# Kernel optimization log

Measured on AMD Instinct MI355X. Metric: run time of the kernel, lower is better.

## Reference

```python
import jax, jax.numpy as jnp
import numpy as np

B, T, D, R = 4, 1024, 512, 64
SLOTS = (1024, 256, 64)
K = 16


def _layernorm(x, g, b, eps=1e-5):
    m = jnp.mean(x, axis=-1, keepdims=True)
    v = jnp.mean(jnp.square(x - m), axis=-1, keepdims=True)
    return (x - m) * jax.lax.rsqrt(v + eps) * g + b


def _signed_softmax(x):
    # signed softmax over the slot axis: sign(x) * softmax(|x|)
    return jnp.sign(x) * jax.nn.softmax(jnp.abs(x), axis=-1)


def _transition_delta(src_val, src_state, dst_val, W, k, n_dst):
    # Low-rank bilinear routing: logits [B, Ns, Nd]
    q = jnp.einsum('bsd,dr->bsr', src_val, W[0])
    kk = jnp.einsum('bnd,dr->bnr', dst_val, W[1])
    logits = jnp.einsum('bsr,bnr->bsn', q, kk) / jnp.sqrt(jnp.float32(W.shape[-1]))
    v, idx = jax.lax.top_k(logits, k)                      # [B, Ns, k]
    w = jnp.sign(v) * jax.nn.softmax(jnp.abs(v), axis=-1)  # signed_abs_softmax over selected edges
    c = w * jax.nn.softplus(src_state)[:, :, None]         # state-weighted edge coefficients [B, Ns, k]
    d = src_val.shape[-1]
    edge_val = (c[..., None] * src_val[:, :, None, :]).reshape(src_val.shape[0], -1, d)
    idx_f = idx.reshape(idx.shape[0], -1)
    cf = c.reshape(c.shape[0], -1)

    def _scatter(i, ev, cc):
        dv = jnp.zeros((n_dst, d), src_val.dtype).at[i].add(ev)
        ds = jnp.zeros((n_dst,), src_val.dtype).at[i].add(cc)
        return ds, dv

    return jax.vmap(_scatter)(idx_f, edge_val, cf)


def _apply_delta(state, val, dstate, dval, g, b):
    # residual merge, then constrain: signed softmax state + LayerNorm values
    return _signed_softmax(state + dstate), _layernorm(val + dval, g, b)


def setup_inputs() -> dict:
    key = jax.random.key(0)
    ks = jax.random.split(key, 20)
    rn = lambda k, s, sc=1.0: jax.random.normal(k, s, jnp.float32) * sc
    return {
        'tok_val': rn(ks[0], (B, T, D)),
        'tok_state': rn(ks[1], (B, T)),
        'mem_state0': rn(ks[2], (B, SLOTS[0]), 0.02),
        'mem_val0': rn(ks[3], (B, SLOTS[0], D), 0.02),
        'mem_state1': rn(ks[4], (B, SLOTS[1]), 0.02),
        'mem_val1': rn(ks[5], (B, SLOTS[1], D), 0.02),
        'mem_state2': rn(ks[6], (B, SLOTS[2]), 0.02),
        'mem_val2': rn(ks[7], (B, SLOTS[2], D), 0.02),
        'write_route': rn(ks[8], (1, 2, D, R), 0.05),
        'prop_route': rn(ks[9], (3, 2, D, R), 0.05),
        'level_route': rn(ks[10], (2, 2, D, R), 0.05),
        'skip_route': rn(ks[11], (2, 2, D, R), 0.05),
        'skip_gates': jnp.full((2,), -1.5, jnp.float32),
        'ln_gamma': jnp.ones((3, D), jnp.float32),
        'ln_beta': jnp.zeros((3, D), jnp.float32),
        'read_route': rn(ks[12], (3, 2, D, R), 0.05),
        'read_proj': rn(ks[13], (3, D, D), 0.02),
        'read_gates': jnp.zeros((3,), jnp.float32),
        'topk': K,
    }


def reference(tok_val, tok_state, mem_state0, mem_val0, mem_state1, mem_val1,
              mem_state2, mem_val2, write_route, prop_route, level_route,
              skip_route, skip_gates, ln_gamma, ln_beta, read_route, read_proj,
              read_gates, topk):
    k = int(topk)
    S0, S1, S2 = mem_state0.shape[1], mem_state1.shape[1], mem_state2.shape[1]

    # --- level 0: token write + pairwise propagation ---
    ds, dv = _transition_delta(tok_val, tok_state, mem_val0, write_route[0], min(k, S0), S0)
    s0, v0 = _apply_delta(mem_state0, mem_val0, ds, dv, ln_gamma[0], ln_beta[0])
    ds, dv = _transition_delta(v0, s0, v0, prop_route[0], min(k, S0), S0)
    s0, v0 = _apply_delta(s0, v0, ds, dv, ln_gamma[0], ln_beta[0])

    # --- level 1: transition from level 0, gated skip from tokens, propagation ---
    ds, dv = _transition_delta(v0, s0, mem_val1, level_route[0], min(k, S1), S1)
    s1, v1 = _apply_delta(mem_state1, mem_val1, ds, dv, ln_gamma[1], ln_beta[1])
    g = jax.nn.sigmoid(skip_gates[0])
    ds, dv = _transition_delta(tok_val, tok_state, v1, skip_route[0], min(k, S1), S1)
    s1, v1 = _apply_delta(s1, v1, g * ds, g * dv, ln_gamma[1], ln_beta[1])
    ds, dv = _transition_delta(v1, s1, v1, prop_route[1], min(k, S1), S1)
    s1, v1 = _apply_delta(s1, v1, ds, dv, ln_gamma[1], ln_beta[1])

    # --- level 2: transition from level 1, gated skip from level 0, propagation ---
    ds, dv = _transition_delta(v1, s1, mem_val2, level_route[1], min(k, S2), S2)
    s2, v2 = _apply_delta(mem_state2, mem_val2, ds, dv, ln_gamma[2], ln_beta[2])
    g = jax.nn.sigmoid(skip_gates[1])
    ds, dv = _transition_delta(v0, s0, v2, skip_route[1], min(k, S2), S2)
    s2, v2 = _apply_delta(s2, v2, g * ds, g * dv, ln_gamma[2], ln_beta[2])
    ds, dv = _transition_delta(v2, s2, v2, prop_route[2], min(k, S2), S2)
    s2, v2 = _apply_delta(s2, v2, ds, dv, ln_gamma[2], ln_beta[2])

    # --- read: tokens attend over each memory level, gated projected residual ---
    out = tok_val
    for l, mv in enumerate((v0, v1, v2)):
        q = jnp.einsum('btd,dr->btr', tok_val, read_route[l, 0])
        kk = jnp.einsum('bnd,dr->bnr', mv, read_route[l, 1])
        logits = jnp.einsum('btr,bnr->btn', q, kk) / jnp.sqrt(jnp.float32(R))
        attn = jax.nn.softmax(logits, axis=-1)
        r = jnp.einsum('btn,bnd->btd', attn, mv)
        out = out + jax.nn.sigmoid(read_gates[l]) * jnp.einsum('btd,de->bte', r, read_proj[l])
    return out
```

## Files before the change

kernel.cpp:

```cpp
#include <hip/hip_runtime.h>
#include <math.h>

typedef __attribute__((ext_vector_type(8))) short short8;
typedef __attribute__((ext_vector_type(4))) float floatx4;

static __device__ __forceinline__ short f2bf(float f) {
    union { float f; unsigned u; } c; c.f = f;
    unsigned r = c.u + 0x7FFF + ((c.u >> 16) & 1);
    return (short)(r >> 16);
}

__launch_bounds__(256)
__global__ void gemm_f32_nt_kernel(const float* __restrict__ A, const float* __restrict__ B,
                                   float* __restrict__ C, int M, int N, int K,
                                   long sA, long sB, long sC, float alpha)
{
    __shared__ float As[32][68];
    __shared__ float Bs[32][68];
    const float* Ab = A + (long)blockIdx.z * sA;
    const float* Bb = B + (long)blockIdx.z * sB;
    float* Cb = C + (long)blockIdx.z * sC;
    int m0 = blockIdx.x * 64, n0 = blockIdx.y * 64;
    int t = threadIdx.x;
    int tx = t & 15, ty = t >> 4;
    float acc[4][4] = {};

    for (int k0 = 0; k0 < K; k0 += 32) {
        {
            int m = t >> 3;
            int kk = (t & 7) * 4;
#pragma unroll
            for (int h = 0; h < 2; ++h) {
                float4 v = *(const float4*)&Ab[(long)(m0 + m + 32 * h) * K + k0 + kk];
                As[kk + 0][m + 32 * h] = v.x; As[kk + 1][m + 32 * h] = v.y;
                As[kk + 2][m + 32 * h] = v.z; As[kk + 3][m + 32 * h] = v.w;
            }
        }
        {
            int n = t >> 3;
            int kk = (t & 7) * 4;
#pragma unroll
            for (int h = 0; h < 2; ++h) {
                float4 v = *(const float4*)&Bb[(long)(n0 + n + 32 * h) * K + k0 + kk];
                Bs[kk + 0][n + 32 * h] = v.x; Bs[kk + 1][n + 32 * h] = v.y;
                Bs[kk + 2][n + 32 * h] = v.z; Bs[kk + 3][n + 32 * h] = v.w;
            }
        }
        __syncthreads();
#pragma unroll 4
        for (int k = 0; k < 32; ++k) {
            float4 a = *(const float4*)&As[k][ty * 4];
            float4 b = *(const float4*)&Bs[k][tx * 4];
            float av[4] = { a.x, a.y, a.z, a.w };
            float bv[4] = { b.x, b.y, b.z, b.w };
#pragma unroll
            for (int i = 0; i < 4; ++i)
#pragma unroll
                for (int j = 0; j < 4; ++j) acc[i][j] += av[i] * bv[j];
        }
        __syncthreads();
    }
#pragma unroll
    for (int i = 0; i < 4; ++i) {
        float4 r;
        r.x = alpha * acc[i][0]; r.y = alpha * acc[i][1];
        r.z = alpha * acc[i][2]; r.w = alpha * acc[i][3];
        *(float4*)&Cb[(long)(m0 + ty * 4 + i) * N + n0 + tx * 4] = r;
    }
}

__launch_bounds__(256)
__global__ void proj_splitk_kernel(const float* __restrict__ Aq, const float* __restrict__ Ak,
                                   const float* __restrict__ Wq, const float* __restrict__ Wk,
                                   float* __restrict__ part,
                                   int Mq, int Mk, long sAq, long sAk, int Bn)
{
    __shared__ float As[32][68];
    __shared__ float Bs[32][68];
    int mqT = Mq >> 6;
    int xt = blockIdx.x, s = blockIdx.y, b = blockIdx.z;
    const float* A; const float* W; int row0, orow;
    if (xt < mqT) { A = Aq + (long)b * sAq; W = Wq; row0 = xt * 64; orow = row0; }
    else { A = Ak + (long)b * sAk; W = Wk; row0 = (xt - mqT) * 64; orow = Mq + row0; }
    int t = threadIdx.x, tx = t & 15, ty = t >> 4;
    float acc[4][4] = {};
    int kbase = s * 64;

    for (int k0 = kbase; k0 < kbase + 64; k0 += 32) {
        {
            int m = t >> 3;
            int kk = (t & 7) * 4;
#pragma unroll
            for (int h = 0; h < 2; ++h) {
                float4 v = *(const float4*)&A[(long)(row0 + m + 32 * h) * 512 + k0 + kk];
                As[kk + 0][m + 32 * h] = v.x; As[kk + 1][m + 32 * h] = v.y;
                As[kk + 2][m + 32 * h] = v.z; As[kk + 3][m + 32 * h] = v.w;
            }
        }
        {
            int kk = t >> 3;
            int nn = (t & 7) * 8;
            float4 v0 = *(const float4*)&W[(long)(k0 + kk) * 64 + nn];
            float4 v1 = *(const float4*)&W[(long)(k0 + kk) * 64 + nn + 4];
            *(float4*)&Bs[kk][nn] = v0;
            *(float4*)&Bs[kk][nn + 4] = v1;
        }
        __syncthreads();
#pragma unroll 4
        for (int k = 0; k < 32; ++k) {
            float4 a = *(const float4*)&As[k][ty * 4];
            float4 b2 = *(const float4*)&Bs[k][tx * 4];
            float av[4] = { a.x, a.y, a.z, a.w };
            float bv[4] = { b2.x, b2.y, b2.z, b2.w };
#pragma unroll
            for (int i = 0; i < 4; ++i)
#pragma unroll
                for (int j = 0; j < 4; ++j) acc[i][j] += av[i] * bv[j];
        }
        __syncthreads();
    }
    long base = ((long)(s * Bn + b) * (Mq + Mk) + orow) * 64;
#pragma unroll
    for (int i = 0; i < 4; ++i)
        *(float4*)&part[base + (long)(ty * 4 + i) * 64 + tx * 4] =
            make_float4(acc[i][0], acc[i][1], acc[i][2], acc[i][3]);
}

__launch_bounds__(256)
__global__ void proj_reduce_kernel(const float* __restrict__ part,
                                   float* __restrict__ qout, float* __restrict__ kout,
                                   int Mq, int Mk, int Bn)
{
    int idx = blockIdx.x * 256 + threadIdx.x;
    int size4b = (Mq + Mk) * 16;
    int total4 = Bn * size4b;
    if (idx >= total4) return;
    const float4* p4 = (const float4*)part;
    long stride4 = (long)total4;
    float4 s = p4[idx];
#pragma unroll
    for (int ss = 1; ss < 8; ++ss) {
        float4 v = p4[ss * stride4 + idx];
        s.x += v.x; s.y += v.y; s.z += v.z; s.w += v.w;
    }
    int b = idx / size4b;
    int rem = idx - b * size4b;
    int r = rem >> 4;
    int c4 = rem & 15;
    if (r < Mq) ((float4*)qout)[((long)b * Mq + r) * 16 + c4] = s;
    else        ((float4*)kout)[((long)b * Mk + (r - Mq)) * 16 + c4] = s;
}

struct ProjDesc {
    const float* A[6];
    const float* W[6];
    long  sA[6];
    int   tileOff[7];
    int   rowOff[6];
    int   Mtot;
};

__launch_bounds__(256)
__global__ void proj_splitk_multi_kernel(ProjDesc d, float* __restrict__ part, int Bn)
{
    __shared__ float As[32][68];
    __shared__ float Bs[32][68];
    int xt = blockIdx.x, s = blockIdx.y, b = blockIdx.z;
    int seg = 0;
    while (xt >= d.tileOff[seg + 1]) ++seg;
    int row0 = (xt - d.tileOff[seg]) * 64;
    const float* A = d.A[seg] + (long)b * d.sA[seg];
    const float* W = d.W[seg];
    int orow = d.rowOff[seg] + row0;
    int t = threadIdx.x, tx = t & 15, ty = t >> 4;
    float acc[4][4] = {};
    int kbase = s * 64;

    for (int k0 = kbase; k0 < kbase + 64; k0 += 32) {
        {
            int m = t >> 3;
            int kk = (t & 7) * 4;
#pragma unroll
            for (int h = 0; h < 2; ++h) {
                float4 v = *(const float4*)&A[(long)(row0 + m + 32 * h) * 512 + k0 + kk];
                As[kk + 0][m + 32 * h] = v.x; As[kk + 1][m + 32 * h] = v.y;
                As[kk + 2][m + 32 * h] = v.z; As[kk + 3][m + 32 * h] = v.w;
            }
        }
        {
            int kk = t >> 3;
            int nn = (t & 7) * 8;
            float4 v0 = *(const float4*)&W[(long)(k0 + kk) * 64 + nn];
            float4 v1 = *(const float4*)&W[(long)(k0 + kk) * 64 + nn + 4];
            *(float4*)&Bs[kk][nn] = v0;
            *(float4*)&Bs[kk][nn + 4] = v1;
        }
        __syncthreads();
#pragma unroll 4
        for (int k = 0; k < 32; ++k) {
            float4 a = *(const float4*)&As[k][ty * 4];
            float4 b2 = *(const float4*)&Bs[k][tx * 4];
            float av[4] = { a.x, a.y, a.z, a.w };
            float bv[4] = { b2.x, b2.y, b2.z, b2.w };
#pragma unroll
            for (int i = 0; i < 4; ++i)
#pragma unroll
                for (int j = 0; j < 4; ++j) acc[i][j] += av[i] * bv[j];
        }
        __syncthreads();
    }
    long base = ((long)(s * Bn + b) * d.Mtot + orow) * 64;
#pragma unroll
    for (int i = 0; i < 4; ++i)
        *(float4*)&part[base + (long)(ty * 4 + i) * 64 + tx * 4] =
            make_float4(acc[i][0], acc[i][1], acc[i][2], acc[i][3]);
}

__launch_bounds__(256)
__global__ void proj_reduce_flat_kernel(const float* __restrict__ part, float* __restrict__ outp,
                                        int total4)
{
    int idx = blockIdx.x * 256 + threadIdx.x;
    if (idx >= total4) return;
    const float4* p4 = (const float4*)part;
    float4 s = p4[idx];
#pragma unroll
    for (int ss = 1; ss < 8; ++ss) {
        float4 v = p4[(long)ss * total4 + idx];
        s.x += v.x; s.y += v.y; s.z += v.z; s.w += v.w;
    }
    ((float4*)outp)[idx] = s;
}

__launch_bounds__(256)
__global__ void gemm_mfma_kernel(const float* __restrict__ A, const unsigned short* __restrict__ Bt,
                                 float* __restrict__ C, int M, int N, int K,
                                 long sA, long sBt, long sC,
                                 float alpha, const float* __restrict__ gate, int gateIdx,
                                 float beta, const float* __restrict__ initC)
{
    __shared__ short As[2048];
    __shared__ short Bs[2048];
    const float* Ab = A + (long)blockIdx.z * sA;
    const unsigned short* Bb = Bt + (long)blockIdx.z * sBt;
    float* Cb = C + (long)blockIdx.z * sC;
    const float* Ib = initC ? initC + (long)blockIdx.z * sC : nullptr;
    int m0 = blockIdx.x * 64, n0 = blockIdx.y * 64;
    int t = threadIdx.x, wave = t >> 6, lane = t & 63;
    int sr = wave * 16 + (lane & 15);
    int sk = (lane >> 4) * 8;
    floatx4 acc[4] = {};

    for (int k0 = 0; k0 < K; k0 += 32) {
        const float* ap = &Ab[(long)(m0 + sr) * K + k0 + sk];
        float4 f0 = *(const float4*)ap;
        float4 f1 = *(const float4*)(ap + 4);
        short8 av;
        av[0] = f2bf(f0.x); av[1] = f2bf(f0.y); av[2] = f2bf(f0.z); av[3] = f2bf(f0.w);
        av[4] = f2bf(f1.x); av[5] = f2bf(f1.y); av[6] = f2bf(f1.z); av[7] = f2bf(f1.w);
        short8 bv = *(const short8*)&Bb[(long)(n0 + sr) * K + k0 + sk];
        ((short8*)As)[t] = av;
        ((short8*)Bs)[t] = bv;
        __syncthreads();
        short8 bf = ((short8*)Bs)[wave * 64 + lane];
#pragma unroll
        for (int mt = 0; mt < 4; ++mt) {
            short8 af = ((short8*)As)[mt * 64 + lane];
            acc[mt] = __builtin_amdgcn_mfma_f32_16x16x32_bf16(af, bf, acc[mt], 0, 0, 0);
        }
        __syncthreads();
    }
    float a = alpha;
    if (gate) a *= 1.f / (1.f + expf(-gate[gateIdx]));
    int col = n0 + wave * 16 + (lane & 15);
#pragma unroll
    for (int mt = 0; mt < 4; ++mt) {
#pragma unroll
        for (int r = 0; r < 4; ++r) {
            int row = m0 + mt * 16 + (lane >> 4) * 4 + r;
            long off = (long)row * N + col;
            float v = a * acc[mt][r];
            if (Ib) v += Ib[off];
            else if (beta != 0.f) v += Cb[off];
            Cb[off] = v;
        }
    }
}

__global__ void transpose_bf16_kernel(const float* __restrict__ in, unsigned short* __restrict__ out,
                                      int Rr, int Cc, long sIn, long sOut)
{
    __shared__ float tile[32][33];
    const float* I = in + (long)blockIdx.z * sIn;
    unsigned short* O = out + (long)blockIdx.z * sOut;
    int c0 = blockIdx.x * 32, r0 = blockIdx.y * 32;
    int tx = threadIdx.x, ty = threadIdx.y;
#pragma unroll
    for (int i = 0; i < 32; i += 8)
        tile[ty + i][tx] = I[(long)(r0 + ty + i) * Cc + c0 + tx];
    __syncthreads();
#pragma unroll
    for (int i = 0; i < 32; i += 8)
        O[(long)(c0 + ty + i) * Rr + r0 + tx] = (unsigned short)f2bf(tile[tx][ty + i]);
}

__global__ void transpose_mv_kernel(const float* __restrict__ mv0, const float* __restrict__ mv1,
                                    const float* __restrict__ mv2,
                                    unsigned short* __restrict__ o0, unsigned short* __restrict__ o1,
                                    unsigned short* __restrict__ o2)
{
    __shared__ float tile[32][33];
    int yt = blockIdx.y;
    const float* in; unsigned short* out; int Nd, r0t;
    if (yt < 32)      { in = mv0; out = o0; Nd = 1024; r0t = yt; }
    else if (yt < 40) { in = mv1; out = o1; Nd = 256;  r0t = yt - 32; }
    else              { in = mv2; out = o2; Nd = 64;   r0t = yt - 40; }
    const float* I = in + (long)blockIdx.z * Nd * 512;
    unsigned short* O = out + (long)blockIdx.z * 512 * Nd;
    int c0 = blockIdx.x * 32, r0 = r0t * 32;
    int tx = threadIdx.x, ty = threadIdx.y;
#pragma unroll
    for (int i = 0; i < 32; i += 8)
        tile[ty + i][tx] = I[(long)(r0 + ty + i) * 512 + c0 + tx];
    __syncthreads();
#pragma unroll
    for (int i = 0; i < 32; i += 8)
        O[(long)(c0 + ty + i) * Nd + r0 + tx] = (unsigned short)f2bf(tile[tx][ty + i]);
}

template<int CNT>
__launch_bounds__(256)
__global__ void topk_coeff_kernel(const float* __restrict__ logits,
                                  const float* __restrict__ state,
                                  int* __restrict__ idx_out, float* __restrict__ c_out,
                                  int* __restrict__ cnt, int nsLog, int Nd)
{
    int wave = threadIdx.x >> 6, lane = threadIdx.x & 63;
    long row = (long)blockIdx.x * 4 + wave;
    const float* L = logits + row * Nd;
    float vreg[CNT];
    if (CNT >= 4) {
#pragma unroll
        for (int q = 0; q < CNT / 4; ++q) {
            float4 v = *(const float4*)&L[lane * CNT + q * 4];
            vreg[q * 4 + 0] = v.x; vreg[q * 4 + 1] = v.y;
            vreg[q * 4 + 2] = v.z; vreg[q * 4 + 3] = v.w;
        }
    } else {
#pragma unroll
        for (int tt = 0; tt < CNT; ++tt) vreg[tt] = L[lane * CNT + tt];
    }

    float m = 0.f, sum = 0.f;
    float myv = 0.f; int myi = 0;
#pragma unroll
    for (int it = 0; it < 16; ++it) {
        float best = -INFINITY; int bidx = 0x7fffffff;
#pragma unroll
        for (int tt = 0; tt < CNT; ++tt) {
            if (vreg[tt] > best) { best = vreg[tt]; bidx = lane * CNT + tt; }
        }
#pragma unroll
        for (int off = 32; off; off >>= 1) {
            float ov = __shfl_down(best, off);
            int   oi = __shfl_down(bidx, off);
            if (ov > best || (ov == best && oi < bidx)) { best = ov; bidx = oi; }
        }
        best = __shfl(best, 0);
        bidx = __shfl(bidx, 0);
        if (it == lane) { myv = best; myi = bidx; }
        float ab = fabsf(best);
        float nm = fmaxf(m, ab);
        sum = sum * expf(m - nm) + expf(ab - nm);
        m = nm;
#pragma unroll
        for (int tt = 0; tt < CNT; ++tt)
            if (lane * CNT + tt == bidx) vreg[tt] = -INFINITY;
    }
    if (lane < 16) {
        float st = state[row];
        float sp = fmaxf(st, 0.f) + log1pf(expf(-fabsf(st)));
        float sgn = (myv > 0.f) ? 1.f : ((myv < 0.f) ? -1.f : 0.f);
        float w = expf(fabsf(myv) - m) / sum;
        c_out[row * 16 + lane] = sgn * w * sp;
        idx_out[row * 16 + lane] = myi;
        int b = (int)(row >> nsLog);
        atomicAdd(&cnt[b * Nd + myi], 1);
    }
}

__launch_bounds__(256)
__global__ void scan_kernel(int* __restrict__ cnt, int* __restrict__ offs, int N)
{
    __shared__ int sums[256];
    int t = threadIdx.x;
    int chunk = N >> 8;
    int base = t * chunk;
    int lc[16];
    int s = 0;
    for (int i = 0; i < chunk; ++i) { lc[i] = cnt[base + i]; s += lc[i]; }
    sums[t] = s;
    __syncthreads();
    for (int off = 1; off < 256; off <<= 1) {
        int v = (t >= off) ? sums[t - off] : 0;
        __syncthreads();
        sums[t] += v;
        __syncthreads();
    }
    int run = sums[t] - s;
    for (int i = 0; i < chunk; ++i) {
        offs[base + i] = run;
        run += lc[i];
        cnt[base + i] = 0;
    }
    if (t == 255) offs[N] = run;
}

__launch_bounds__(256)
__global__ void fill_edges_kernel(const int* __restrict__ idx, const int* __restrict__ offs,
                                  int* __restrict__ cursor, int* __restrict__ elist,
                                  int nsShift, int Nd, int E)
{
    int e = blockIdx.x * 256 + threadIdx.x;
    if (e >= E) return;
    int b = e >> nsShift;
    int d = b * Nd + idx[e];
    int pos = offs[d] + atomicAdd(&cursor[d], 1);
    elist[pos] = e;
}

#define ECHUNK 512
__launch_bounds__(256)
__global__ void gather_ln_kernel(const float* __restrict__ src_val, const float* __restrict__ c,
                                 const int* __restrict__ elist, const int* __restrict__ offs,
                                 const float* __restrict__ v_in, float* __restrict__ v_out,
                                 float* __restrict__ ds, int* __restrict__ cursor,
                                 const float* __restrict__ gamma, const float* __restrict__ beta,
                                 const float* __restrict__ gatePtr, int gateIdx, int nsShift)
{
    __shared__ float sc[ECHUNK];
    __shared__ int   srow[ECHUNK];
    __shared__ float part[4][512];
    __shared__ float pcs[4];
    __shared__ float red[4];
    long row = blockIdx.x;
    int t = threadIdx.x, w = t >> 6, lane = t & 63;
    int e0 = offs[row], e1 = offs[row + 1];
    int mask = (1 << nsShift) - 1;
    int cb = lane * 8;
    float a[8] = {};
    float cs = 0.f;
    float gate = 1.f;
    if (gatePtr) gate = 1.f / (1.f + expf(-gatePtr[gateIdx]));

    for (int cstart = e0; cstart < e1; cstart += ECHUNK) {
        int cnt = min(e1 - cstart, ECHUNK);
        for (int i = t; i < cnt; i += 256) {
            int e = elist[cstart + i];
            sc[i] = c[e];
            int b = e >> nsShift;
            int s = (e & mask) >> 4;
            srow[i] = (b << (nsShift - 4)) + s;
        }
        __syncthreads();
        int j = w;
        for (; j + 12 < cnt; j += 16) {
            float c0 = sc[j], c1 = sc[j + 4], c2 = sc[j + 8], c3 = sc[j + 12];
            const float* p0 = src_val + ((long)srow[j]      << 9) + cb;
            const float* p1 = src_val + ((long)srow[j + 4]  << 9) + cb;
            const float* p2 = src_val + ((long)srow[j + 8]  << 9) + cb;
            const float* p3 = src_val + ((long)srow[j + 12] << 9) + cb;
            float4 x00 = *(const float4*)p0,       x01 = *(const float4*)(p0 + 4);
            float4 x10 = *(const float4*)p1,       x11 = *(const float4*)(p1 + 4);
            float4 x20 = *(const float4*)p2,       x21 = *(const float4*)(p2 + 4);
            float4 x30 = *(const float4*)p3,       x31 = *(const float4*)(p3 + 4);
            a[0] += c0 * x00.x + c1 * x10.x + c2 * x20.x + c3 * x30.x;
            a[1] += c0 * x00.y + c1 * x10.y + c2 * x20.y + c3 * x30.y;
            a[2] += c0 * x00.z + c1 * x10.z + c2 * x20.z + c3 * x30.z;
            a[3] += c0 * x00.w + c1 * x10.w + c2 * x20.w + c3 * x30.w;
            a[4] += c0 * x01.x + c1 * x11.x + c2 * x21.x + c3 * x31.x;
            a[5] += c0 * x01.y + c1 * x11.y + c2 * x21.y + c3 * x31.y;
            a[6] += c0 * x01.z + c1 * x11.z + c2 * x21.z + c3 * x31.z;
            a[7] += c0 * x01.w + c1 * x11.w + c2 * x21.w + c3 * x31.w;
            cs += c0 + c1 + c2 + c3;
        }
        for (; j < cnt; j += 4) {
            float cv = sc[j];
            const float* p = src_val + ((long)srow[j] << 9) + cb;
            float4 x0 = *(const float4*)p, x1 = *(const float4*)(p + 4);
            a[0] += cv * x0.x; a[1] += cv * x0.y; a[2] += cv * x0.z; a[3] += cv * x0.w;
            a[4] += cv * x1.x; a[5] += cv * x1.y; a[6] += cv * x1.z; a[7] += cv * x1.w;
            cs += cv;
        }
        __syncthreads();
    }
#pragma unroll
    for (int i = 0; i < 8; ++i) part[w][cb + i] = a[i];
    if (lane == 0) pcs[w] = cs;
    __syncthreads();
    float r0 = part[0][t] + part[1][t] + part[2][t] + part[3][t];
    float r1 = part[0][t + 256] + part[1][t + 256] + part[2][t + 256] + part[3][t + 256];
    if (t == 0) { ds[row] = pcs[0] + pcs[1] + pcs[2] + pcs[3]; cursor[row] = 0; }

    const float* vi = v_in + (row << 9);
    float x0 = vi[t]       + gate * r0;
    float x1 = vi[t + 256] + gate * r1;
    float s = x0 + x1;
    for (int off = 32; off; off >>= 1) s += __shfl_down(s, off);
    if ((t & 63) == 0) red[t >> 6] = s;
    __syncthreads();
    float mean = (red[0] + red[1] + red[2] + red[3]) * (1.f / 512.f);
    float d0 = x0 - mean, d1 = x1 - mean;
    float ss = d0 * d0 + d1 * d1;
    for (int off = 32; off; off >>= 1) ss += __shfl_down(ss, off);
    __syncthreads();
    if ((t & 63) == 0) red[t >> 6] = ss;
    __syncthreads();
    float var = (red[0] + red[1] + red[2] + red[3]) * (1.f / 512.f);
    float rstd = rsqrtf(var + 1e-5f);
    float* vo = v_out + (row << 9);
    vo[t]       = d0 * rstd * gamma[t]       + beta[t];
    vo[t + 256] = d1 * rstd * gamma[t + 256] + beta[t + 256];
}

__launch_bounds__(256)
__global__ void apply_state_kernel(const float* __restrict__ s_in, const float* __restrict__ ds,
                                   float* __restrict__ s_out, int Nd,
                                   const float* __restrict__ gatePtr, int gateIdx)
{
    __shared__ float sh[1024];
    __shared__ float red[4];
    int b = blockIdx.x, t = threadIdx.x;
    float gate = 1.f;
    if (gatePtr) gate = 1.f / (1.f + expf(-gatePtr[gateIdx]));
    float lmax = 0.f;
    for (int i = t; i < Nd; i += 256) {
        float x = s_in[b * Nd + i] + gate * ds[b * Nd + i];
        sh[i] = x;
        lmax = fmaxf(lmax, fabsf(x));
    }
    for (int off = 32; off; off >>= 1) lmax = fmaxf(lmax, __shfl_down(lmax, off));
    if ((t & 63) == 0) red[t >> 6] = lmax;
    __syncthreads();
    float bmax = fmaxf(fmaxf(red[0], red[1]), fmaxf(red[2], red[3]));
    float lsum = 0.f;
    for (int i = t; i < Nd; i += 256) lsum += expf(fabsf(sh[i]) - bmax);
    for (int off = 32; off; off >>= 1) lsum += __shfl_down(lsum, off);
    __syncthreads();
    if ((t & 63) == 0) red[t >> 6] = lsum;
    __syncthreads();
    float inv = 1.f / (red[0] + red[1] + red[2] + red[3]);
    for (int i = t; i < Nd; i += 256) {
        float x = sh[i];
        float sgn = (x > 0.f) ? 1.f : ((x < 0.f) ? -1.f : 0.f);
        s_out[b * Nd + i] = sgn * expf(fabsf(x) - bmax) * inv;
    }
}

__launch_bounds__(256)
__global__ void softmax_rows_kernel(float* __restrict__ logits, int Nd)
{
    __shared__ float red[4];
    long row = blockIdx.x;
    int t = threadIdx.x;
    float* L = logits + row * (long)Nd;
    float lmax = -INFINITY;
    for (int i = t; i < Nd; i += 256) lmax = fmaxf(lmax, L[i]);
    for (int off = 32; off; off >>= 1) lmax = fmaxf(lmax, __shfl_down(lmax, off));
    if ((t & 63) == 0) red[t >> 6] = lmax;
    __syncthreads();
    float bmax = fmaxf(fmaxf(red[0], red[1]), fmaxf(red[2], red[3]));
    float lsum = 0.f;
    for (int i = t; i < Nd; i += 256) lsum += expf(L[i] - bmax);
    for (int off = 32; off; off >>= 1) lsum += __shfl_down(lsum, off);
    __syncthreads();
    if ((t & 63) == 0) red[t >> 6] = lsum;
    __syncthreads();
    float inv = 1.f / (red[0] + red[1] + red[2] + red[3]);
    for (int i = t; i < Nd; i += 256) L[i] = expf(L[i] - bmax) * inv;
}

extern "C" void kernel_launch(void* const* d_in, const int* in_sizes, int n_in,
                              void* d_out, int out_size, void* d_ws, size_t ws_size,
                              hipStream_t stream)
{
    const int Bn = 4, T = 1024, D = 512, R = 64;
    const int S0 = 1024, S1 = 256, S2 = 64;
    const long RT = (long)D * R;
    const int MR = 3 * T + S0 + S1 + S2;

    const float* tok_val    = (const float*)d_in[0];
    const float* tok_state  = (const float*)d_in[1];
    const float* mem_state0 = (const float*)d_in[2];
    const float* mem_val0   = (const float*)d_in[3];
    const float* mem_state1 = (const float*)d_in[4];
    const float* mem_val1   = (const float*)d_in[5];
    const float* mem_state2 = (const float*)d_in[6];
    const float* mem_val2   = (const float*)d_in[7];
    const float* write_route= (const float*)d_in[8];
    const float* prop_route = (const float*)d_in[9];
    const float* level_route= (const float*)d_in[10];
    const float* skip_route = (const float*)d_in[11];
    const float* skip_gates = (const float*)d_in[12];
    const float* ln_gamma   = (const float*)d_in[13];
    const float* ln_beta    = (const float*)d_in[14];
    const float* read_route = (const float*)d_in[15];
    const float* read_proj  = (const float*)d_in[16];
    const float* read_gates = (const float*)d_in[17];
    float* out = (float*)d_out;

    float* p = (float*)d_ws;
    float* v0  = p; p += (long)Bn * S0 * D;
    float* v0b = p; p += (long)Bn * S0 * D;
    float* s0  = p; p += Bn * S0;
    float* v1  = p; p += (long)Bn * S1 * D;
    float* v1b = p; p += (long)Bn * S1 * D;
    float* s1  = p; p += Bn * S1;
    float* v2  = p; p += (long)Bn * S2 * D;
    float* v2b = p; p += (long)Bn * S2 * D;
    float* s2  = p; p += Bn * S2;
    float* qb  = p; p += (long)Bn * T * R;
    float* kb  = p; p += (long)Bn * S0 * R;
    float* rqk = p; p += (long)Bn * MR * R;
    float* lb  = p; p += (long)Bn * T * S0;
    float* cbuf= p; p += (long)Bn * T * 16;
    int*   ib  = (int*)p; p += (long)Bn * T * 16;
    float* dsb = p; p += Bn * S0;
    float* rb  = p; p += (long)Bn * T * D;
    int* cntb  = (int*)p; p += Bn * S0;
    int* curb  = (int*)p; p += Bn * S0;
    int* offsb = (int*)p; p += Bn * S0 + 1;
    int* elistb= (int*)p; p += (long)Bn * T * 16;
    unsigned short* projT = (unsigned short*)p; p += (3 * (long)D * D) / 2 + 4;
    unsigned short* mvT0  = (unsigned short*)p; p += ((long)Bn * D * S0) / 2 + 4;
    unsigned short* mvT1  = (unsigned short*)p; p += ((long)Bn * D * S1) / 2 + 4;
    unsigned short* mvT2  = (unsigned short*)p; p += ((long)Bn * D * S2) / 2 + 4;
    float* partb = p; p += 8L * Bn * MR * R;

    auto proj = [&](const float* Aq, const float* Ak, const float* Wq, const float* Wk,
                    int Mq, int Mk, long sAq, long sAk, float* qout, float* kout) {
        proj_splitk_kernel<<<dim3((Mq + Mk) / 64, 8, Bn), 256, 0, stream>>>(
            Aq, Ak, Wq, Wk, partb, Mq, Mk, sAq, sAk, Bn);
        int total4 = Bn * (Mq + Mk) * 16;
        proj_reduce_kernel<<<(total4 + 255) / 256, 256, 0, stream>>>(
            partb, qout, kout, Mq, Mk, Bn);
    };

    hipMemsetAsync(cntb, 0, (size_t)2 * Bn * S0 * sizeof(int), stream);

    auto trans = [&](const float* sv, const float* ss, const float* dval,
                     const float* W, int Ns, int Nd,
                     const float* v_in, float* v_out, const float* sin, float* sout,
                     int lvl, const float* gptr, int gidx) {
        proj(sv, dval, W, W + RT, Ns, Nd, (long)Ns * D, (long)Nd * D, qb, kb);
        gemm_f32_nt_kernel<<<dim3(Ns / 64, Nd / 64, Bn), 256, 0, stream>>>(
            qb, kb, lb, Ns, Nd, R, (long)Ns * R, (long)Nd * R, (long)Ns * Nd, 0.125f);
        int nsLog = 31 - __builtin_clz((unsigned)Ns);
        int nsShift = nsLog + 4;
        int rowBlocks = Bn * Ns / 4;
        if (Nd == 1024)
            topk_coeff_kernel<16><<<rowBlocks, 256, 0, stream>>>(lb, ss, ib, cbuf, cntb, nsLog, Nd);
        else if (Nd == 256)
            topk_coeff_kernel<4><<<rowBlocks, 256, 0, stream>>>(lb, ss, ib, cbuf, cntb, nsLog, Nd);
        else
            topk_coeff_kernel<1><<<rowBlocks, 256, 0, stream>>>(lb, ss, ib, cbuf, cntb, nsLog, Nd);
        int E = Bn * Ns * 16;
        scan_kernel<<<1, 256, 0, stream>>>(cntb, offsb, Bn * Nd);
        fill_edges_kernel<<<(E + 255) / 256, 256, 0, stream>>>(ib, offsb, curb, elistb,
                                                               nsShift, Nd, E);
        gather_ln_kernel<<<Bn * Nd, 256, 0, stream>>>(sv, cbuf, elistb, offsb,
                                                      v_in, v_out, dsb, curb,
                                                      ln_gamma + lvl * D, ln_beta + lvl * D,
                                                      gptr, gidx, nsShift);
        apply_state_kernel<<<Bn, 256, 0, stream>>>(sin, dsb, sout, Nd, gptr, gidx);
    };

    trans(tok_val, tok_state, mem_val0, write_route, T, S0,
          mem_val0, v0, mem_state0, s0, 0, nullptr, 0);
    trans(v0, s0, v0, prop_route + 0 * 2 * RT, S0, S0,
          v0, v0b, s0, s0, 0, nullptr, 0);

    trans(v0b, s0, mem_val1, level_route + 0 * 2 * RT, S0, S1,
          mem_val1, v1, mem_state1, s1, 1, nullptr, 0);
    trans(tok_val, tok_state, v1, skip_route + 0 * 2 * RT, T, S1,
          v1, v1, s1, s1, 1, skip_gates, 0);
    trans(v1, s1, v1, prop_route + 1 * 2 * RT, S1, S1,
          v1, v1b, s1, s1, 1, nullptr, 0);

    trans(v1b, s1, mem_val2, level_route + 1 * 2 * RT, S1, S2,
          mem_val2, v2, mem_state2, s2, 2, nullptr, 0);
    trans(v0b, s0, v2, skip_route + 1 * 2 * RT, S0, S2,
          v2, v2, s2, s2, 2, skip_gates, 1);
    trans(v2, s2, v2, prop_route + 2 * 2 * RT, S2, S2,
          v2, v2b, s2, s2, 2, nullptr, 0);

    transpose_bf16_kernel<<<dim3(D / 32, D / 32, 3), dim3(32, 8), 0, stream>>>(
        read_proj, projT, D, D, (long)D * D, (long)D * D);
    transpose_mv_kernel<<<dim3(D / 32, (S0 + S1 + S2) / 32, Bn), dim3(32, 8), 0, stream>>>(
        v0b, v1b, v2b, mvT0, mvT1, mvT2);

    {
        ProjDesc d = {};
        const float* mvs[3] = { v0b, v1b, v2b };
        const int nds[3] = { S0, S1, S2 };
        int tiles = 0, roff = 0;
        for (int l = 0; l < 3; ++l) {
            d.A[l] = tok_val; d.W[l] = read_route + (long)l * 2 * RT;
            d.sA[l] = (long)T * D; d.rowOff[l] = roff;
            d.tileOff[l] = tiles; tiles += T / 64; roff += T;
        }
        for (int l = 0; l < 3; ++l) {
            d.A[3 + l] = mvs[l]; d.W[3 + l] = read_route + (long)l * 2 * RT + RT;
            d.sA[3 + l] = (long)nds[l] * D; d.rowOff[3 + l] = roff;
            d.tileOff[3 + l] = tiles; tiles += nds[l] / 64; roff += nds[l];
        }
        d.tileOff[6] = tiles;
        d.Mtot = MR;
        proj_splitk_multi_kernel<<<dim3(tiles, 8, Bn), 256, 0, stream>>>(d, partb, Bn);
        int total4 = Bn * MR * 16;
        proj_reduce_flat_kernel<<<(total4 + 255) / 256, 256, 0, stream>>>(partb, rqk, total4);
    }

    const unsigned short* mvTs[3] = { mvT0, mvT1, mvT2 };
    const int nds[3] = { S0, S1, S2 };
    int koff = 3 * T;
    for (int l = 0; l < 3; ++l) {
        int Nd = nds[l];
        gemm_f32_nt_kernel<<<dim3(T / 64, Nd / 64, Bn), 256, 0, stream>>>(
            rqk + (long)l * T * R, rqk + (long)koff * R, lb, T, Nd, R,
            (long)MR * R, (long)MR * R, (long)T * Nd, 0.125f);
        koff += Nd;
        softmax_rows_kernel<<<Bn * T, 256, 0, stream>>>(lb, Nd);
        gemm_mfma_kernel<<<dim3(T / 64, D / 64, Bn), 256, 0, stream>>>(
            lb, mvTs[l], rb, T, D, Nd, (long)T * Nd, (long)D * Nd, (long)T * D,
            1.f, nullptr, 0, 0.f, nullptr);
        gemm_mfma_kernel<<<dim3(T / 64, D / 64, Bn), 256, 0, stream>>>(
            rb, projT + (long)l * D * D, out, T, D, D,
            (long)T * D, 0, (long)T * D, 1.f, read_gates, l,
            1.f, (l == 0) ? tok_val : nullptr);
    }
}
```

Baseline: 909.0 us.

## Batch read-phase levels into segmented kernels and one concatenated projection GEMM

The per-level read loop of logits GEMM, softmax, attention GEMM and projection GEMM is replaced by single segmented launches covering all three memory levels. The attention outputs are concatenated along the feature axis, and the three gated projections are folded into one K=1536 GEMM whose weights are pre-scaled by the sigmoid gates. This cuts kernel launches and the read-modify-write accumulation into the output. It needs separate logits buffers per level and a larger concatenated intermediate, and the attention kernel has unbalanced work per block because K differs across levels.

```diff
diff --git a/kernel.cpp b/kernel.cpp
--- a/kernel.cpp
+++ b/kernel.cpp
@@ -65,6 +65,78 @@
         float4 r;
         r.x = alpha * acc[i][0]; r.y = alpha * acc[i][1];
         r.z = alpha * acc[i][2]; r.w = alpha * acc[i][3];
+        *(float4*)&Cb[(long)(m0 + ty * 4 + i) * N + n0 + tx * 4] = r;
+    }
+}
+
+struct LogitsSeg {
+    const float* A[3];
+    const float* B[3];
+    float* C[3];
+    long sC[3];
+    int Nd[3];
+    int yOff[4];
+    long sAB;
+};
+
+__launch_bounds__(256)
+__global__ void gemm_logits_seg_kernel(LogitsSeg d)
+{
+    __shared__ float As[32][68];
+    __shared__ float Bs[32][68];
+    int yt = blockIdx.y;
+    int seg = 0;
+    while (yt >= d.yOff[seg + 1]) ++seg;
+    int n0 = (yt - d.yOff[seg]) * 64;
+    const float* Ab = d.A[seg] + (long)blockIdx.z * d.sAB;
+    const float* Bb = d.B[seg] + (long)blockIdx.z * d.sAB;
+    float* Cb = d.C[seg] + (long)blockIdx.z * d.sC[seg];
+    int N = d.Nd[seg];
+    int m0 = blockIdx.x * 64;
+    int t = threadIdx.x, tx = t & 15, ty = t >> 4;
+    float acc[4][4] = {};
+    const int K = 64;
+
+    for (int k0 = 0; k0 < K; k0 += 32) {
+        {
+            int m = t >> 3;
+            int kk = (t & 7) * 4;
+#pragma unroll
+            for (int h = 0; h < 2; ++h) {
+                float4 v = *(const float4*)&Ab[(long)(m0 + m + 32 * h) * K + k0 + kk];
+                As[kk + 0][m + 32 * h] = v.x; As[kk + 1][m + 32 * h] = v.y;
+                As[kk + 2][m + 32 * h] = v.z; As[kk + 3][m + 32 * h] = v.w;
+            }
+        }
+        {
+            int n = t >> 3;
+            int kk = (t & 7) * 4;
+#pragma unroll
+            for (int h = 0; h < 2; ++h) {
+                float4 v = *(const float4*)&Bb[(long)(n0 + n + 32 * h) * K + k0 + kk];
+                Bs[kk + 0][n + 32 * h] = v.x; Bs[kk + 1][n + 32 * h] = v.y;
+                Bs[kk + 2][n + 32 * h] = v.z; Bs[kk + 3][n + 32 * h] = v.w;
+            }
+        }
+        __syncthreads();
+#pragma unroll 4
+        for (int k = 0; k < 32; ++k) {
+            float4 a = *(const float4*)&As[k][ty * 4];
+            float4 b = *(const float4*)&Bs[k][tx * 4];
+            float av[4] = { a.x, a.y, a.z, a.w };
+            float bv[4] = { b.x, b.y, b.z, b.w };
+#pragma unroll
+            for (int i = 0; i < 4; ++i)
+#pragma unroll
+                for (int j = 0; j < 4; ++j) acc[i][j] += av[i] * bv[j];
+        }
+        __syncthreads();
+    }
+#pragma unroll
+    for (int i = 0; i < 4; ++i) {
+        float4 r;
+        r.x = 0.125f * acc[i][0]; r.y = 0.125f * acc[i][1];
+        r.z = 0.125f * acc[i][2]; r.w = 0.125f * acc[i][3];
         *(float4*)&Cb[(long)(m0 + ty * 4 + i) * N + n0 + tx * 4] = r;
     }
 }
@@ -236,8 +308,7 @@
 __global__ void gemm_mfma_kernel(const float* __restrict__ A, const unsigned short* __restrict__ Bt,
                                  float* __restrict__ C, int M, int N, int K,
                                  long sA, long sBt, long sC,
-                                 float alpha, const float* __restrict__ gate, int gateIdx,
-                                 float beta, const float* __restrict__ initC)
+                                 float alpha, const float* __restrict__ initC)
 {
     __shared__ short As[2048];
     __shared__ short Bs[2048];
@@ -270,8 +341,6 @@
         }
         __syncthreads();
     }
-    float a = alpha;
-    if (gate) a *= 1.f / (1.f + expf(-gate[gateIdx]));
     int col = n0 + wave * 16 + (lane & 15);
 #pragma unroll
     for (int mt = 0; mt < 4; ++mt) {
@@ -279,29 +348,85 @@
         for (int r = 0; r < 4; ++r) {
             int row = m0 + mt * 16 + (lane >> 4) * 4 + r;
             long off = (long)row * N + col;
-            float v = a * acc[mt][r];
+            float v = alpha * acc[mt][r];
             if (Ib) v += Ib[off];
-            else if (beta != 0.f) v += Cb[off];
             Cb[off] = v;
         }
     }
 }
 
-__global__ void transpose_bf16_kernel(const float* __restrict__ in, unsigned short* __restrict__ out,
-                                      int Rr, int Cc, long sIn, long sOut)
+struct AttnSeg {
+    const float* A[3];
+    const unsigned short* Bt[3];
+    int K[3];
+    long sA[3], sBt[3];
+};
+
+__launch_bounds__(256)
+__global__ void gemm_mfma_attn_seg_kernel(AttnSeg d, float* __restrict__ rcat, long sC)
+{
+    __shared__ short As[2048];
+    __shared__ short Bs[2048];
+    int lvl = blockIdx.x >> 4;
+    int m0 = (blockIdx.x & 15) * 64;
+    int n0 = blockIdx.y * 64;
+    int K = d.K[lvl];
+    const float* Ab = d.A[lvl] + (long)blockIdx.z * d.sA[lvl];
+    const unsigned short* Bb = d.Bt[lvl] + (long)blockIdx.z * d.sBt[lvl];
+    float* Cb = rcat + (long)blockIdx.z * sC + lvl * 512;
+    int t = threadIdx.x, wave = t >> 6, lane = t & 63;
+    int sr = wave * 16 + (lane & 15);
+    int sk = (lane >> 4) * 8;
+    floatx4 acc[4] = {};
+
+    for (int k0 = 0; k0 < K; k0 += 32) {
+        const float* ap = &Ab[(long)(m0 + sr) * K + k0 + sk];
+        float4 f0 = *(const float4*)ap;
+        float4 f1 = *(const float4*)(ap + 4);
+        short8 av;
+        av[0] = f2bf(f0.x); av[1] = f2bf(f0.y); av[2] = f2bf(f0.z); av[3] = f2bf(f0.w);
+        av[4] = f2bf(f1.x); av[5] = f2bf(f1.y); av[6] = f2bf(f1.z); av[7] = f2bf(f1.w);
+        short8 bv = *(const short8*)&Bb[(long)(n0 + sr) * K + k0 + sk];
+        ((short8*)As)[t] = av;
+        ((short8*)Bs)[t] = bv;
+        __syncthreads();
+        short8 bf = ((short8*)Bs)[wave * 64 + lane];
+#pragma unroll
+        for (int mt = 0; mt < 4; ++mt) {
+            short8 af = ((short8*)As)[mt * 64 + lane];
+            acc[mt] = __builtin_amdgcn_mfma_f32_16x16x32_bf16(af, bf, acc[mt], 0, 0, 0);
+        }
+        __syncthreads();
+    }
+    int col = n0 + wave * 16 + (lane & 15);
+#pragma unroll
+    for (int mt = 0; mt < 4; ++mt) {
+#pragma unroll
+        for (int r = 0; r < 4; ++r) {
+            int row = m0 + mt * 16 + (lane >> 4) * 4 + r;
+            Cb[(long)row * 1536 + col] = acc[mt][r];
+        }
+    }
+}
+
+__global__ void transpose_proj_gated_kernel(const float* __restrict__ proj,
+                                            const float* __restrict__ gates,
+                                            unsigned short* __restrict__ outp)
 {
     __shared__ float tile[32][33];
-    const float* I = in + (long)blockIdx.z * sIn;
-    unsigned short* O = out + (long)blockIdx.z * sOut;
-    int c0 = blockIdx.x * 32, r0 = blockIdx.y * 32;
+    int l = blockIdx.z;
+    float g = 1.f / (1.f + expf(-gates[l]));
+    const float* I = proj + (long)l * 512 * 512;
+    int n0 = blockIdx.x * 32, d0 = blockIdx.y * 32;
     int tx = threadIdx.x, ty = threadIdx.y;
 #pragma unroll
     for (int i = 0; i < 32; i += 8)
-        tile[ty + i][tx] = I[(long)(r0 + ty + i) * Cc + c0 + tx];
+        tile[ty + i][tx] = I[(long)(d0 + ty + i) * 512 + n0 + tx];
     __syncthreads();
 #pragma unroll
     for (int i = 0; i < 32; i += 8)
-        O[(long)(c0 + ty + i) * Rr + r0 + tx] = (unsigned short)f2bf(tile[tx][ty + i]);
+        outp[(long)(n0 + ty + i) * 1536 + l * 512 + d0 + tx] =
+            (unsigned short)f2bf(g * tile[tx][ty + i]);
 }
 
 __global__ void transpose_mv_kernel(const float* __restrict__ mv0, const float* __restrict__ mv1,
@@ -558,12 +683,16 @@
 }
 
 __launch_bounds__(256)
-__global__ void softmax_rows_kernel(float* __restrict__ logits, int Nd)
+__global__ void softmax_seg_kernel(float* __restrict__ lb0, float* __restrict__ lb1,
+                                   float* __restrict__ lb2)
 {
     __shared__ float red[4];
+    int lvl = blockIdx.y;
+    int Nd = (lvl == 0) ? 1024 : (lvl == 1) ? 256 : 64;
+    float* base = (lvl == 0) ? lb0 : (lvl == 1) ? lb1 : lb2;
     long row = blockIdx.x;
     int t = threadIdx.x;
-    float* L = logits + row * (long)Nd;
+    float* L = base + row * (long)Nd;
     float lmax = -INFINITY;
     for (int i = t; i < Nd; i += 256) lmax = fmaxf(lmax, L[i]);
     for (int off = 32; off; off >>= 1) lmax = fmaxf(lmax, __shfl_down(lmax, off));
@@ -622,16 +751,18 @@
     float* qb  = p; p += (long)Bn * T * R;
     float* kb  = p; p += (long)Bn * S0 * R;
     float* rqk = p; p += (long)Bn * MR * R;
-    float* lb  = p; p += (long)Bn * T * S0;
+    float* lb0 = p; p += (long)Bn * T * S0;
+    float* lb1 = p; p += (long)Bn * T * S1;
+    float* lb2 = p; p += (long)Bn * T * S2;
     float* cbuf= p; p += (long)Bn * T * 16;
     int*   ib  = (int*)p; p += (long)Bn * T * 16;
     float* dsb = p; p += Bn * S0;
-    float* rb  = p; p += (long)Bn * T * D;
+    float* rcat= p; p += (long)Bn * T * 1536;
     int* cntb  = (int*)p; p += Bn * S0;
     int* curb  = (int*)p; p += Bn * S0;
     int* offsb = (int*)p; p += Bn * S0 + 1;
     int* elistb= (int*)p; p += (long)Bn * T * 16;
-    unsigned short* projT = (unsigned short*)p; p += (3 * (long)D * D) / 2 + 4;
+    unsigned short* pcatT = (unsigned short*)p; p += (512L * 1536) / 2 + 4;
     unsigned short* mvT0  = (unsigned short*)p; p += ((long)Bn * D * S0) / 2 + 4;
     unsigned short* mvT1  = (unsigned short*)p; p += ((long)Bn * D * S1) / 2 + 4;
     unsigned short* mvT2  = (unsigned short*)p; p += ((long)Bn * D * S2) / 2 + 4;
@@ -654,16 +785,16 @@
                      int lvl, const float* gptr, int gidx) {
         proj(sv, dval, W, W + RT, Ns, Nd, (long)Ns * D, (long)Nd * D, qb, kb);
         gemm_f32_nt_kernel<<<dim3(Ns / 64, Nd / 64, Bn), 256, 0, stream>>>(
-            qb, kb, lb, Ns, Nd, R, (long)Ns * R, (long)Nd * R, (long)Ns * Nd, 0.125f);
+            qb, kb, lb0, Ns, Nd, R, (long)Ns * R, (long)Nd * R, (long)Ns * Nd, 0.125f);
         int nsLog = 31 - __builtin_clz((unsigned)Ns);
         int nsShift = nsLog + 4;
         int rowBlocks = Bn * Ns / 4;
         if (Nd == 1024)
-            topk_coeff_kernel<16><<<rowBlocks, 256, 0, stream>>>(lb, ss, ib, cbuf, cntb, nsLog, Nd);
+            topk_coeff_kernel<16><<<rowBlocks, 256, 0, stream>>>(lb0, ss, ib, cbuf, cntb, nsLog, Nd);
         else if (Nd == 256)
-            topk_coeff_kernel<4><<<rowBlocks, 256, 0, stream>>>(lb, ss, ib, cbuf, cntb, nsLog, Nd);
+            topk_coeff_kernel<4><<<rowBlocks, 256, 0, stream>>>(lb0, ss, ib, cbuf, cntb, nsLog, Nd);
         else
-            topk_coeff_kernel<1><<<rowBlocks, 256, 0, stream>>>(lb, ss, ib, cbuf, cntb, nsLog, Nd);
+            topk_coeff_kernel<1><<<rowBlocks, 256, 0, stream>>>(lb0, ss, ib, cbuf, cntb, nsLog, Nd);
         int E = Bn * Ns * 16;
         scan_kernel<<<1, 256, 0, stream>>>(cntb, offsb, Bn * Nd);
         fill_edges_kernel<<<(E + 255) / 256, 256, 0, stream>>>(ib, offsb, curb, elistb,
@@ -694,8 +825,8 @@
     trans(v2, s2, v2, prop_route + 2 * 2 * RT, S2, S2,
           v2, v2b, s2, s2, 2, nullptr, 0);
 
-    transpose_bf16_kernel<<<dim3(D / 32, D / 32, 3), dim3(32, 8), 0, stream>>>(
-        read_proj, projT, D, D, (long)D * D, (long)D * D);
+    transpose_proj_gated_kernel<<<dim3(D / 32, D / 32, 3), dim3(32, 8), 0, stream>>>(
+        read_proj, read_gates, pcatT);
     transpose_mv_kernel<<<dim3(D / 32, (S0 + S1 + S2) / 32, Bn), dim3(32, 8), 0, stream>>>(
         v0b, v1b, v2b, mvT0, mvT1, mvT2);
 
@@ -721,22 +852,45 @@
         proj_reduce_flat_kernel<<<(total4 + 255) / 256, 256, 0, stream>>>(partb, rqk, total4);
     }
 
-    const unsigned short* mvTs[3] = { mvT0, mvT1, mvT2 };
-    const int nds[3] = { S0, S1, S2 };
-    int koff = 3 * T;
-    for (int l = 0; l < 3; ++l) {
-        int Nd = nds[l];
-        gemm_f32_nt_kernel<<<dim3(T / 64, Nd / 64, Bn), 256, 0, stream>>>(
-            rqk + (long)l * T * R, rqk + (long)koff * R, lb, T, Nd, R,
-            (long)MR * R, (long)MR * R, (long)T * Nd, 0.125f);
-        koff += Nd;
-        softmax_rows_kernel<<<Bn * T, 256, 0, stream>>>(lb, Nd);
-        gemm_mfma_kernel<<<dim3(T / 64, D / 64, Bn), 256, 0, stream>>>(
-            lb, mvTs[l], rb, T, D, Nd, (long)T * Nd, (long)D * Nd, (long)T * D,
-            1.f, nullptr, 0, 0.f, nullptr);
-        gemm_mfma_kernel<<<dim3(T / 64, D / 64, Bn), 256, 0, stream>>>(
-            rb, projT + (long)l * D * D, out, T, D, D,
-            (long)T * D, 0, (long)T * D, 1.f, read_gates, l,
-            1.f, (l == 0) ? tok_val : nullptr);
-    }
-}
+    {
+        LogitsSeg d = {};
+        float* lbs[3] = { lb0, lb1, lb2 };
+        const int nds[3] = { S0, S1, S2 };
+        int koff = 3 * T, yo = 0;
+        for (int l = 0; l < 3; ++l) {
+            d.A[l] = rqk + (long)l * T * R;
+            d.B[l] = rqk + (long)koff * R;
+            d.C[l] = lbs[l];
+            d.sC[l] = (long)T * nds[l];
+            d.Nd[l] = nds[l];
+            d.yOff[l] = yo;
+            yo += nds[l] / 64;
+            koff += nds[l];
+        }
+        d.yOff[3] = yo;
+        d.sAB = (long)MR * R;
+        gemm_logits_seg_kernel<<<dim3(T / 64, yo, Bn), 256, 0, stream>>>(d);
+    }
+
+    softmax_seg_kernel<<<dim3(Bn * T, 3), 256, 0, stream>>>(lb0, lb1, lb2);
+
+    {
+        AttnSeg d = {};
+        float* lbs[3] = { lb0, lb1, lb2 };
+        const unsigned short* mvTs[3] = { mvT0, mvT1, mvT2 };
+        const int nds[3] = { S0, S1, S2 };
+        for (int l = 0; l < 3; ++l) {
+            d.A[l] = lbs[l];
+            d.Bt[l] = mvTs[l];
+            d.K[l] = nds[l];
+            d.sA[l] = (long)T * nds[l];
+            d.sBt[l] = (long)D * nds[l];
+        }
+        gemm_mfma_attn_seg_kernel<<<dim3(48, D / 64, Bn), 256, 0, stream>>>(
+            d, rcat, (long)T * 1536);
+    }
+
+    gemm_mfma_kernel<<<dim3(T / 64, D / 64, Bn), 256, 0, stream>>>(
+        rcat, pcatT, out, T, D, 1536,
+        (long)T * 1536, 0, (long)T * D, 1.f, tok_val);
+}
```

Result: faster. 868.4 us (-4.5%).
